# Performance work log

Measured on AMD Instinct MI355X. Metric: run time of the kernel, lower is better.

Reference implementation:

```python
import jax, jax.numpy as jnp
import numpy as np

E = 1_000_000
F = 16   # input_node_features_size
H = 32   # input_node_hidden_state_size
OUT = 64 # output_edge_hidden_state_size
IN = 2 * (F + H) + 1       # 97
MID = (2 * (F + H) + OUT) // 2  # 80


def setup_inputs() -> dict:
    key = jax.random.key(0)
    ks = jax.random.split(key, 9)
    inp = {
        "dst_node_feat": jax.random.normal(ks[0], (E, F), jnp.float32),
        "dst_node_hidden": jax.random.normal(ks[1], (E, H), jnp.float32),
        "src_node_feat": jax.random.normal(ks[2], (E, F), jnp.float32),
        "src_node_hidden": jax.random.normal(ks[3], (E, H), jnp.float32),
        "edge_feat": jax.random.normal(ks[4], (E,), jnp.float32),
        # Linear layer params (torch layout: W [out, in])
        "W1": jax.random.normal(ks[5], (MID, IN), jnp.float32) * (1.0 / np.sqrt(IN)),
        "b1": jax.random.normal(ks[6], (MID,), jnp.float32) * 0.01,
        "W2": jax.random.normal(ks[7], (OUT, MID), jnp.float32) * (1.0 / np.sqrt(MID)),
        "b2": jax.random.normal(ks[8], (OUT,), jnp.float32) * 0.01,
    }
    return inp


def reference(dst_node_feat, dst_node_hidden, src_node_feat, src_node_hidden,
              edge_feat, W1, b1, W2, b2):
    # concat [dst_feat, dst_hidden, src_feat, src_hidden, edge_feat[:, None]] -> [E, IN]
    x = jnp.concatenate(
        [dst_node_feat, dst_node_hidden, src_node_feat, src_node_hidden,
         edge_feat[:, None]], axis=1)
    # Linear -> Dropout(eval=identity) -> ReLU -> Linear -> Tanh
    h = jax.nn.relu(x @ W1.T + b1)           # [E, MID]
    out = jnp.tanh(h @ W2.T + b2)            # [E, OUT]
    return out
```

## Files before the change

kernel.cpp:

```cpp
#include <hip/hip_runtime.h>
#include <stdint.h>


typedef float  f32x4  __attribute__((ext_vector_type(4)));
typedef short  short8 __attribute__((ext_vector_type(8)));

#define LDSPAD 104

__device__ __forceinline__ unsigned short f2bf(float f) {
  union { float f; unsigned u; } v; v.f = f;
  unsigned r = v.u + 0x7FFFu + ((v.u >> 16) & 1u);
  return (unsigned short)(r >> 16);
}

__global__ __launch_bounds__(256, 3)
void edge_net_kernel(const float* __restrict__ dstf,
                     const float* __restrict__ dsth,
                     const float* __restrict__ srcf,
                     const float* __restrict__ srch,
                     const float* __restrict__ ef,
                     const float* __restrict__ W1,
                     const float* __restrict__ b1,
                     const float* __restrict__ W2,
                     const float* __restrict__ b2,
                     float* __restrict__ out,
                     int nTiles) {
  __shared__ unsigned short w1s[80 * LDSPAD];
  __shared__ unsigned short w2s[64 * LDSPAD];
  __shared__ unsigned short hs [64 * LDSPAD];
  __shared__ float w1last[80];
  __shared__ float b1s[80];
  __shared__ float b2s[64];

  const int tid = threadIdx.x;

  for (int idx = tid; idx < 80 * 96; idx += 256) {
    int n = idx / 96, k = idx - n * 96;
    w1s[n * LDSPAD + k] = f2bf(W1[n * 97 + k]);
  }
  for (int idx = tid; idx < 64 * 96; idx += 256) {
    int n = idx / 96, k = idx - n * 96;
    w2s[n * LDSPAD + k] = (k < 80) ? f2bf(W2[n * 80 + k]) : (unsigned short)0;
  }
  for (int idx = tid; idx < 64 * LDSPAD; idx += 256) hs[idx] = 0;
  if (tid < 80) { w1last[tid] = W1[tid * 97 + 96]; b1s[tid] = b1[tid]; }
  if (tid < 64) { b2s[tid] = b2[tid]; }
  __syncthreads();

  const int wave = tid >> 6;
  const int lane = tid & 63;
  const int m    = lane & 15;
  const int quad = lane >> 4;

  float bias1[5], wl[5], bias2[4];
  #pragma unroll
  for (int i = 0; i < 5; ++i) { bias1[i] = b1s[i * 16 + m]; wl[i] = w1last[i * 16 + m]; }
  #pragma unroll
  for (int j = 0; j < 4; ++j) bias2[j] = b2s[j * 16 + m];

  for (int tile = blockIdx.x; tile < nTiles; tile += gridDim.x) {
    const int eb = tile * 64 + wave * 16;
    const int e  = eb + m;

    f32x4 xa[3][2];
    #pragma unroll
    for (int t = 0; t < 3; ++t) {
      const int c = t * 4 + quad;
      const float* p;
      if (c < 2)      p = dstf + e * 16 + c * 8;
      else if (c < 6) p = dsth + e * 32 + (c - 2) * 8;
      else if (c < 8) p = srcf + e * 16 + (c - 6) * 8;
      else            p = srch + e * 32 + (c - 8) * 8;
      xa[t][0] = *(const f32x4*)p;
      xa[t][1] = *(const f32x4*)(p + 4);
    }
    const f32x4 ef4 = *(const f32x4*)(ef + eb + quad * 4);

    short8 af[3];
    #pragma unroll
    for (int t = 0; t < 3; ++t) {
      #pragma unroll
      for (int j = 0; j < 4; ++j) {
        af[t][j]     = (short)f2bf(xa[t][0][j]);
        af[t][4 + j] = (short)f2bf(xa[t][1][j]);
      }
    }

    f32x4 acc1[5];
    #pragma unroll
    for (int i = 0; i < 5; ++i) acc1[i] = (f32x4){bias1[i], bias1[i], bias1[i], bias1[i]};
    #pragma unroll
    for (int t = 0; t < 3; ++t) {
      #pragma unroll
      for (int i = 0; i < 5; ++i) {
        short8 bfr = *(const short8*)&w1s[(i * 16 + m) * LDSPAD + t * 32 + quad * 8];
        acc1[i] = __builtin_amdgcn_mfma_f32_16x16x32_bf16(af[t], bfr, acc1[i], 0, 0, 0);
      }
    }

    #pragma unroll
    for (int i = 0; i < 5; ++i) {
      #pragma unroll
      for (int r = 0; r < 4; ++r) {
        float h = fmaxf(fmaf(ef4[r], wl[i], acc1[i][r]), 0.0f);
        hs[(wave * 16 + quad * 4 + r) * LDSPAD + i * 16 + m] = f2bf(h);
      }
    }
    asm volatile("" ::: "memory");

    short8 hf[3];
    #pragma unroll
    for (int t = 0; t < 3; ++t)
      hf[t] = *(const short8*)&hs[(wave * 16 + m) * LDSPAD + t * 32 + quad * 8];
    asm volatile("" ::: "memory");

    f32x4 acc2[4];
    #pragma unroll
    for (int j = 0; j < 4; ++j) acc2[j] = (f32x4){bias2[j], bias2[j], bias2[j], bias2[j]};
    #pragma unroll
    for (int t = 0; t < 3; ++t) {
      #pragma unroll
      for (int j = 0; j < 4; ++j) {
        short8 bfr = *(const short8*)&w2s[(j * 16 + m) * LDSPAD + t * 32 + quad * 8];
        acc2[j] = __builtin_amdgcn_mfma_f32_16x16x32_bf16(hf[t], bfr, acc2[j], 0, 0, 0);
      }
    }

    #pragma unroll
    for (int j = 0; j < 4; ++j) {
      #pragma unroll
      for (int r = 0; r < 4; ++r) {
        float y  = acc2[j][r];
        float ex = __builtin_amdgcn_exp2f(y * 2.885390081777927f);
        float th = 1.0f - 2.0f * __builtin_amdgcn_rcpf(ex + 1.0f);
        out[(eb + quad * 4 + r) * 64 + j * 16 + m] = th;
      }
    }
  }
}

extern "C" void kernel_launch(void* const* d_in, const int* in_sizes, int n_in,
                              void* d_out, int out_size, void* d_ws, size_t ws_size,
                              hipStream_t stream) {
  const float* dstf = (const float*)d_in[0];
  const float* dsth = (const float*)d_in[1];
  const float* srcf = (const float*)d_in[2];
  const float* srch = (const float*)d_in[3];
  const float* ef   = (const float*)d_in[4];
  const float* W1   = (const float*)d_in[5];
  const float* b1   = (const float*)d_in[6];
  const float* W2   = (const float*)d_in[7];
  const float* b2   = (const float*)d_in[8];
  float* out = (float*)d_out;

  const int E = in_sizes[4];
  const int nTiles = E >> 6;
  int grid = 768;
  if (grid > nTiles) grid = nTiles;

  hipLaunchKernelGGL(edge_net_kernel, dim3(grid), dim3(256), 0, stream,
                     dstf, dsth, srcf, srch, ef, W1, b1, W2, b2, out, nTiles);
}
```

Before: 524.0 us.

## Software-pipeline input loads and enlarge blocks to 512 threads

Prefetches the next tile's input rows into registers before running the current tile's MFMAs, so global load latency overlaps with compute. Blocks grow to 8 waves covering 128 edges, and the grid becomes 512 blocks with bounds checks against E. The bf16 conversion is simplified to round-half-up and packed two values per perm instruction, and the edge-feature term is folded into the accumulator init. In exchange it uses more registers for the prefetch buffers and slightly changes rounding.

```diff
diff --git a/kernel.cpp b/kernel.cpp
--- a/kernel.cpp
+++ b/kernel.cpp
@@ -4,16 +4,21 @@
 
 typedef float  f32x4  __attribute__((ext_vector_type(4)));
 typedef short  short8 __attribute__((ext_vector_type(8)));
+typedef unsigned int u32;
 
 #define LDSPAD 104
 
 __device__ __forceinline__ unsigned short f2bf(float f) {
   union { float f; unsigned u; } v; v.f = f;
-  unsigned r = v.u + 0x7FFFu + ((v.u >> 16) & 1u);
-  return (unsigned short)(r >> 16);
+  return (unsigned short)((v.u + 0x8000u) >> 16);
 }
 
-__global__ __launch_bounds__(256, 3)
+__device__ __forceinline__ u32 pk2(float lo, float hi) {
+  union { float f; u32 u; } a, b; a.f = lo; b.f = hi;
+  return __builtin_amdgcn_perm(b.u + 0x8000u, a.u + 0x8000u, 0x07060302u);
+}
+
+__global__ __launch_bounds__(512, 4)
 void edge_net_kernel(const float* __restrict__ dstf,
                      const float* __restrict__ dsth,
                      const float* __restrict__ srcf,
@@ -24,25 +29,25 @@
                      const float* __restrict__ W2,
                      const float* __restrict__ b2,
                      float* __restrict__ out,
-                     int nTiles) {
+                     int nT2, int E) {
   __shared__ unsigned short w1s[80 * LDSPAD];
   __shared__ unsigned short w2s[64 * LDSPAD];
-  __shared__ unsigned short hs [64 * LDSPAD];
+  __shared__ unsigned short hs [128 * LDSPAD];
   __shared__ float w1last[80];
   __shared__ float b1s[80];
   __shared__ float b2s[64];
 
   const int tid = threadIdx.x;
 
-  for (int idx = tid; idx < 80 * 96; idx += 256) {
+  for (int idx = tid; idx < 80 * 96; idx += 512) {
     int n = idx / 96, k = idx - n * 96;
     w1s[n * LDSPAD + k] = f2bf(W1[n * 97 + k]);
   }
-  for (int idx = tid; idx < 64 * 96; idx += 256) {
+  for (int idx = tid; idx < 64 * 96; idx += 512) {
     int n = idx / 96, k = idx - n * 96;
     w2s[n * LDSPAD + k] = (k < 80) ? f2bf(W2[n * 80 + k]) : (unsigned short)0;
   }
-  for (int idx = tid; idx < 64 * LDSPAD; idx += 256) hs[idx] = 0;
+  for (int idx = tid; idx < 128 * LDSPAD; idx += 512) hs[idx] = 0;
   if (tid < 80) { w1last[tid] = W1[tid * 97 + 96]; b1s[tid] = b1[tid]; }
   if (tid < 64) { b2s[tid] = b2[tid]; }
   __syncthreads();
@@ -58,85 +63,110 @@
   #pragma unroll
   for (int j = 0; j < 4; ++j) bias2[j] = b2s[j * 16 + m];
 
-  for (int tile = blockIdx.x; tile < nTiles; tile += gridDim.x) {
-    const int eb = tile * 64 + wave * 16;
-    const int e  = eb + m;
+  const int grid = gridDim.x;
+  int tile = blockIdx.x;
 
-    f32x4 xa[3][2];
-    #pragma unroll
-    for (int t = 0; t < 3; ++t) {
-      const int c = t * 4 + quad;
-      const float* p;
-      if (c < 2)      p = dstf + e * 16 + c * 8;
-      else if (c < 6) p = dsth + e * 32 + (c - 2) * 8;
-      else if (c < 8) p = srcf + e * 16 + (c - 6) * 8;
-      else            p = srch + e * 32 + (c - 8) * 8;
-      xa[t][0] = *(const f32x4*)p;
-      xa[t][1] = *(const f32x4*)(p + 4);
-    }
-    const f32x4 ef4 = *(const f32x4*)(ef + eb + quad * 4);
+  f32x4 xa[3][2];
+  f32x4 ef4;
 
-    short8 af[3];
-    #pragma unroll
-    for (int t = 0; t < 3; ++t) {
+#define LOADX(EB) do {                                        \
+    const int e_ = (EB) + m;                                  \
+    _Pragma("unroll")                                         \
+    for (int t_ = 0; t_ < 3; ++t_) {                          \
+      const int c_ = t_ * 4 + quad;                           \
+      const float* p_;                                        \
+      if (c_ < 2)      p_ = dstf + e_ * 16 + c_ * 8;          \
+      else if (c_ < 6) p_ = dsth + e_ * 32 + (c_ - 2) * 8;    \
+      else if (c_ < 8) p_ = srcf + e_ * 16 + (c_ - 6) * 8;    \
+      else             p_ = srch + e_ * 32 + (c_ - 8) * 8;    \
+      xa[t_][0] = *(const f32x4*)p_;                          \
+      xa[t_][1] = *(const f32x4*)(p_ + 4);                    \
+    }                                                         \
+    ef4 = *(const f32x4*)(ef + (EB) + quad * 4);              \
+  } while (0)
+
+  int  eb  = tile * 128 + wave * 16;
+  bool act = (tile < nT2) && (eb < E);
+  if (act) LOADX(eb);
+
+  for (; tile < nT2; tile += grid) {
+    const int e0 = tile * 128 + wave * 16;
+
+    union { short8 s; u32 u[4]; } af[3];
+    f32x4 acc1[5];
+    if (act) {
       #pragma unroll
-      for (int j = 0; j < 4; ++j) {
-        af[t][j]     = (short)f2bf(xa[t][0][j]);
-        af[t][4 + j] = (short)f2bf(xa[t][1][j]);
+      for (int t = 0; t < 3; ++t) {
+        af[t].u[0] = pk2(xa[t][0][0], xa[t][0][1]);
+        af[t].u[1] = pk2(xa[t][0][2], xa[t][0][3]);
+        af[t].u[2] = pk2(xa[t][1][0], xa[t][1][1]);
+        af[t].u[3] = pk2(xa[t][1][2], xa[t][1][3]);
+      }
+      #pragma unroll
+      for (int i = 0; i < 5; ++i) {
+        #pragma unroll
+        for (int r = 0; r < 4; ++r) acc1[i][r] = fmaf(ef4[r], wl[i], bias1[i]);
       }
     }
 
-    f32x4 acc1[5];
-    #pragma unroll
-    for (int i = 0; i < 5; ++i) acc1[i] = (f32x4){bias1[i], bias1[i], bias1[i], bias1[i]};
-    #pragma unroll
-    for (int t = 0; t < 3; ++t) {
+    const int  tn   = tile + grid;
+    const int  ebn  = tn * 128 + wave * 16;
+    const bool actn = (ebn < E);
+    if (actn) LOADX(ebn);
+
+    if (act) {
+      #pragma unroll
+      for (int t = 0; t < 3; ++t) {
+        #pragma unroll
+        for (int i = 0; i < 5; ++i) {
+          short8 bfr = *(const short8*)&w1s[(i * 16 + m) * LDSPAD + t * 32 + quad * 8];
+          acc1[i] = __builtin_amdgcn_mfma_f32_16x16x32_bf16(af[t].s, bfr, acc1[i], 0, 0, 0);
+        }
+      }
+
       #pragma unroll
       for (int i = 0; i < 5; ++i) {
-        short8 bfr = *(const short8*)&w1s[(i * 16 + m) * LDSPAD + t * 32 + quad * 8];
-        acc1[i] = __builtin_amdgcn_mfma_f32_16x16x32_bf16(af[t], bfr, acc1[i], 0, 0, 0);
+        #pragma unroll
+        for (int r = 0; r < 4; ++r) {
+          float h = fmaxf(acc1[i][r], 0.0f);
+          hs[(wave * 16 + quad * 4 + r) * LDSPAD + i * 16 + m] = f2bf(h);
+        }
+      }
+      asm volatile("" ::: "memory");
+
+      short8 hf[3];
+      #pragma unroll
+      for (int t = 0; t < 3; ++t)
+        hf[t] = *(const short8*)&hs[(wave * 16 + m) * LDSPAD + t * 32 + quad * 8];
+      asm volatile("" ::: "memory");
+
+      f32x4 acc2[4];
+      #pragma unroll
+      for (int j = 0; j < 4; ++j) acc2[j] = (f32x4){bias2[j], bias2[j], bias2[j], bias2[j]};
+      #pragma unroll
+      for (int t = 0; t < 3; ++t) {
+        #pragma unroll
+        for (int j = 0; j < 4; ++j) {
+          short8 bfr = *(const short8*)&w2s[(j * 16 + m) * LDSPAD + t * 32 + quad * 8];
+          acc2[j] = __builtin_amdgcn_mfma_f32_16x16x32_bf16(hf[t], bfr, acc2[j], 0, 0, 0);
+        }
+      }
+
+      #pragma unroll
+      for (int j = 0; j < 4; ++j) {
+        #pragma unroll
+        for (int r = 0; r < 4; ++r) {
+          float y  = acc2[j][r];
+          float ex = __builtin_amdgcn_exp2f(y * 2.885390081777927f);
+          float th = 1.0f - 2.0f * __builtin_amdgcn_rcpf(ex + 1.0f);
+          out[(e0 + quad * 4 + r) * 64 + j * 16 + m] = th;
+        }
       }
     }
 
-    #pragma unroll
-    for (int i = 0; i < 5; ++i) {
-      #pragma unroll
-      for (int r = 0; r < 4; ++r) {
-        float h = fmaxf(fmaf(ef4[r], wl[i], acc1[i][r]), 0.0f);
-        hs[(wave * 16 + quad * 4 + r) * LDSPAD + i * 16 + m] = f2bf(h);
-      }
-    }
-    asm volatile("" ::: "memory");
-
-    short8 hf[3];
-    #pragma unroll
-    for (int t = 0; t < 3; ++t)
-      hf[t] = *(const short8*)&hs[(wave * 16 + m) * LDSPAD + t * 32 + quad * 8];
-    asm volatile("" ::: "memory");
-
-    f32x4 acc2[4];
-    #pragma unroll
-    for (int j = 0; j < 4; ++j) acc2[j] = (f32x4){bias2[j], bias2[j], bias2[j], bias2[j]};
-    #pragma unroll
-    for (int t = 0; t < 3; ++t) {
-      #pragma unroll
-      for (int j = 0; j < 4; ++j) {
-        short8 bfr = *(const short8*)&w2s[(j * 16 + m) * LDSPAD + t * 32 + quad * 8];
-        acc2[j] = __builtin_amdgcn_mfma_f32_16x16x32_bf16(hf[t], bfr, acc2[j], 0, 0, 0);
-      }
-    }
-
-    #pragma unroll
-    for (int j = 0; j < 4; ++j) {
-      #pragma unroll
-      for (int r = 0; r < 4; ++r) {
-        float y  = acc2[j][r];
-        float ex = __builtin_amdgcn_exp2f(y * 2.885390081777927f);
-        float th = 1.0f - 2.0f * __builtin_amdgcn_rcpf(ex + 1.0f);
-        out[(eb + quad * 4 + r) * 64 + j * 16 + m] = th;
-      }
-    }
+    act = actn;
   }
+#undef LOADX
 }
 
 extern "C" void kernel_launch(void* const* d_in, const int* in_sizes, int n_in,
@@ -153,11 +183,11 @@
   const float* b2   = (const float*)d_in[8];
   float* out = (float*)d_out;
 
-  const int E = in_sizes[4];
-  const int nTiles = E >> 6;
-  int grid = 768;
-  if (grid > nTiles) grid = nTiles;
+  const int E   = in_sizes[4];
+  const int nT2 = (E + 127) >> 7;
+  int grid = 512;
+  if (grid > nT2) grid = nT2;
 
-  hipLaunchKernelGGL(edge_net_kernel, dim3(grid), dim3(256), 0, stream,
-                     dstf, dsth, srcf, srch, ef, W1, b1, W2, b2, out, nTiles);
+  hipLaunchKernelGGL(edge_net_kernel, dim3(grid), dim3(512), 0, stream,
+                     dstf, dsth, srcf, srch, ef, W1, b1, W2, b2, out, nT2, E);
 }
```

Result: slower. 561.2 us (+7.1%).
